# Kernel optimization log

Hardware: AMD Instinct MI355X
Metric: run time of the kernel (lower is better)

Reference implementation:

```python
import jax, jax.numpy as jnp
import numpy as np

N = 50000        # number of nodes
K = 32           # sampled neighbors per node (fixed degree)
D = 128          # input_dim
DOUT = 128       # output_dim


def setup_inputs() -> dict:
    key = jax.random.key(0)
    k1, k2, k3, k4, k5 = jax.random.split(key, 5)
    node_fea1 = jax.random.normal(k1, (N, D), dtype=jnp.float32)
    node_fea2 = jax.random.normal(k2, (N, D), dtype=jnp.float32)
    neigh_idx1 = jax.random.randint(k3, (N, K), 0, N, dtype=jnp.int32)
    neigh_idx2 = jax.random.randint(k4, (N, K), 0, N, dtype=jnp.int32)
    # xavier-uniform init for weight [4*D, DOUT]
    limit = float(np.sqrt(6.0 / (4 * D + DOUT)))
    weight = jax.random.uniform(k5, (4 * D, DOUT), dtype=jnp.float32,
                                minval=-limit, maxval=limit)
    return {"node_fea1": node_fea1, "node_fea2": node_fea2,
            "neigh_idx1": neigh_idx1, "neigh_idx2": neigh_idx2,
            "weight": weight}


def reference(node_fea1, node_fea2, neigh_idx1, neigh_idx2, weight):
    # neighbor mean aggregation of node_fea1 over the two neighbor lists
    # (forward_den reads node_fea1 in BOTH aggregation blocks)
    nei1 = node_fea1[neigh_idx1].mean(axis=1)   # [N, D]
    nei2 = node_fea1[neigh_idx2].mean(axis=1)   # [N, D]
    cat_fea = jnp.concatenate([node_fea1, node_fea2, nei1, nei2], axis=1)  # [N, 4D]
    return jnp.tanh(cat_fea @ weight)           # [N, DOUT]
```

## Files before the change

### kernel.cpp

```cpp
#include <hip/hip_runtime.h>
#include <math.h>

#define N_NODES 50000
#define KNEI    32
#define DIM     128
#define DOUT    128
#define NUNITS  (2 * N_NODES)

typedef __attribute__((ext_vector_type(8))) short short8;
typedef __attribute__((ext_vector_type(4))) float floatx4;

static __device__ __forceinline__ unsigned short f2bf(float f) {
    unsigned int u = __float_as_uint(f);
    unsigned int lsb = (u >> 16) & 1u;
    u += 0x7fffu + lsb;
    return (unsigned short)(u >> 16);
}
static __device__ __forceinline__ unsigned int pack2(float a, float b) {
    return (unsigned int)f2bf(a) | ((unsigned int)f2bf(b) << 16);
}
static __device__ __forceinline__ float fast_tanh(float x) {
    float ax = fabsf(x);
    float e  = __expf(2.0f * ax);
    float t  = 1.0f - 2.0f / (e + 1.0f);
    return copysignf(t, x);
}
static __device__ __forceinline__ unsigned int pk4_i8(float a, float b, float c,
                                                      float d, float inv) {
    int qa = (int)rintf(a * inv) & 0xff;
    int qb = (int)rintf(b * inv) & 0xff;
    int qc = (int)rintf(c * inv) & 0xff;
    int qd = (int)rintf(d * inv) & 0xff;
    return (unsigned int)(qa | (qb << 8) | (qc << 16) | (qd << 24));
}


__global__ __launch_bounds__(256) void convert_i8(
    const float* __restrict__ src, unsigned int* __restrict__ Q8,
    float* __restrict__ Sc)
{
    int t = blockIdx.x * 256 + threadIdx.x;
    if (t >= N_NODES * 8) return;
    int node = t >> 3, j = t & 7;
    const float* rp = src + node * DIM + j * 16;
    float4 v0 = *(const float4*)rp;
    float4 v1 = *(const float4*)(rp + 4);
    float4 v2 = *(const float4*)(rp + 8);
    float4 v3 = *(const float4*)(rp + 12);

    float am = fabsf(v0.x);
    am = fmaxf(am, fabsf(v0.y)); am = fmaxf(am, fabsf(v0.z)); am = fmaxf(am, fabsf(v0.w));
    am = fmaxf(am, fabsf(v1.x)); am = fmaxf(am, fabsf(v1.y));
    am = fmaxf(am, fabsf(v1.z)); am = fmaxf(am, fabsf(v1.w));
    am = fmaxf(am, fabsf(v2.x)); am = fmaxf(am, fabsf(v2.y));
    am = fmaxf(am, fabsf(v2.z)); am = fmaxf(am, fabsf(v2.w));
    am = fmaxf(am, fabsf(v3.x)); am = fmaxf(am, fabsf(v3.y));
    am = fmaxf(am, fabsf(v3.z)); am = fmaxf(am, fabsf(v3.w));
    #pragma unroll
    for (int d = 1; d < 8; d <<= 1) am = fmaxf(am, __shfl_xor(am, d, 64));

    float inv = (am > 1e-30f) ? 127.0f / am : 0.0f;
    int4 o;
    o.x = (int)pk4_i8(v0.x, v0.y, v0.z, v0.w, inv);
    o.y = (int)pk4_i8(v1.x, v1.y, v1.z, v1.w, inv);
    o.z = (int)pk4_i8(v2.x, v2.y, v2.z, v2.w, inv);
    o.w = (int)pk4_i8(v3.x, v3.y, v3.z, v3.w, inv);
    *(int4*)(Q8 + node * 32 + j * 4) = o;
    if (j == 0) Sc[node] = am * (1.0f / 127.0f);
}

__global__ __launch_bounds__(256) void transpose_w(
    const float* __restrict__ W, unsigned short* __restrict__ Wt)
{
    int t = blockIdx.x * 256 + threadIdx.x;
    int k = t >> 7, n = t & 127;
    Wt[n * 512 + k] = f2bf(W[t]);
}

__global__ __launch_bounds__(256) void aggregate_i8(
    const unsigned char* __restrict__ Q8,
    const float* __restrict__ Sc,
    const int* __restrict__ idx1,
    const int* __restrict__ idx2,
    unsigned short* __restrict__ NEI)
{
    __shared__ int   idxs[32][32];
    __shared__ float scs[32][32];

    const int tid = threadIdx.x;
    const int bu0 = blockIdx.x * 32;
    const int ul  = tid >> 3;
    const int l   = tid & 7;

    {
        int uu = bu0 + ul;
        const int* ip = ((uu & 1) ? idx2 : idx1) + (uu >> 1) * KNEI + l * 4;
        int4 v = *(const int4*)ip;
        *(int4*)&idxs[ul][l * 4] = v;
    }
    __syncthreads();

    {
        #pragma unroll
        for (int k = 0; k < 4; ++k)
            scs[ul][l * 4 + k] = Sc[idxs[ul][l * 4 + k]];
    }
    __syncthreads();

    const int u    = bu0 + ul;
    const int node = u >> 1;
    const int list = u & 1;

    int4 I[8];
    #pragma unroll
    for (int q = 0; q < 8; ++q) I[q] = *(const int4*)&idxs[ul][q * 4];

    const unsigned char* base = Q8 + l * 16;
    float sums[16];
    #pragma unroll
    for (int i = 0; i < 16; ++i) sums[i] = 0.f;

    #pragma unroll
    for (int q = 0; q < 8; ++q) {
        int rows[4] = {I[q].x, I[q].y, I[q].z, I[q].w};
        #pragma unroll
        for (int t4 = 0; t4 < 4; ++t4) {
            int4 v = *(const int4*)(base + (size_t)rows[t4] * 128);
            float s = scs[ul][q * 4 + t4];
            int d[4] = {v.x, v.y, v.z, v.w};
            #pragma unroll
            for (int j = 0; j < 4; ++j) {
                int w = d[j];
                sums[4 * j + 0] = fmaf(s, (float)((w << 24) >> 24), sums[4 * j + 0]);
                sums[4 * j + 1] = fmaf(s, (float)((w << 16) >> 24), sums[4 * j + 1]);
                sums[4 * j + 2] = fmaf(s, (float)((w <<  8) >> 24), sums[4 * j + 2]);
                sums[4 * j + 3] = fmaf(s, (float)( w        >> 24), sums[4 * j + 3]);
            }
        }
    }

    const float invK = 1.0f / 32.0f;
    int4 o0, o1;
    o0.x = (int)pack2(sums[0] * invK,  sums[1] * invK);
    o0.y = (int)pack2(sums[2] * invK,  sums[3] * invK);
    o0.z = (int)pack2(sums[4] * invK,  sums[5] * invK);
    o0.w = (int)pack2(sums[6] * invK,  sums[7] * invK);
    o1.x = (int)pack2(sums[8] * invK,  sums[9] * invK);
    o1.y = (int)pack2(sums[10] * invK, sums[11] * invK);
    o1.z = (int)pack2(sums[12] * invK, sums[13] * invK);
    o1.w = (int)pack2(sums[14] * invK, sums[15] * invK);
    unsigned short* op = NEI + node * 256 + list * 128 + l * 16;
    *(int4*)op       = o0;
    *(int4*)(op + 8) = o1;
}

__global__ __launch_bounds__(256) void gemm128(
    const float*          __restrict__ fea1,
    const float*          __restrict__ fea2,
    const unsigned short* __restrict__ NEI,
    const unsigned short* __restrict__ Wt,
    float* __restrict__ out)
{
    __shared__ unsigned short As[128][72];
    __shared__ unsigned short Bs[128][72];

    const int tid  = threadIdx.x;
    const int w    = tid >> 6;
    const int lane = tid & 63;
    const int m0   = blockIdx.x * 128;
    const int wm   = (w & 1) * 64;
    const int wn   = (w >> 1) * 64;
    const int lm   = lane & 15;
    const int lk   = (lane >> 4) * 8;

    floatx4 acc[4][4];
    #pragma unroll
    for (int i = 0; i < 4; ++i)
        #pragma unroll
        for (int j = 0; j < 4; ++j)
            acc[i][j] = (floatx4){0.f, 0.f, 0.f, 0.f};

    for (int cc = 0; cc < 8; ++cc) {
        const int kb = cc * 64;
        if (cc < 4) {
            const float* src = (cc < 2) ? fea1 : fea2;
            const int cbase = (cc & 1) * 64;
            #pragma unroll
            for (int i = 0; i < 8; ++i) {
                int f   = tid + i * 256;
                int row = f >> 4;
                int c4  = (f & 15) * 4;
                int node = m0 + row;
                if (node >= N_NODES) node = N_NODES - 1;
                float4 v = *(const float4*)(src + node * DIM + cbase + c4);
                *(unsigned int*)&As[row][c4 + 0] = pack2(v.x, v.y);
                *(unsigned int*)&As[row][c4 + 2] = pack2(v.z, v.w);
            }
        } else {
            const int cb = kb - 256;
            #pragma unroll
            for (int i = 0; i < 4; ++i) {
                int sl  = tid + i * 256;
                int row = sl >> 3;
                int o8  = (sl & 7) * 8;
                int node = m0 + row;
                if (node >= N_NODES) node = N_NODES - 1;
                *(int4*)&As[row][o8] = *(const int4*)(NEI + node * 256 + cb + o8);
            }
        }
        #pragma unroll
        for (int i = 0; i < 4; ++i) {
            int sl  = tid + i * 256;
            int row = sl >> 3;
            int o8  = (sl & 7) * 8;
            *(int4*)&Bs[row][o8] = *(const int4*)(Wt + row * 512 + kb + o8);
        }
        __syncthreads();

        #pragma unroll
        for (int ks = 0; ks < 64; ks += 32) {
            short8 af[4], bf_[4];
            #pragma unroll
            for (int im = 0; im < 4; ++im)
                af[im] = *(const short8*)&As[wm + im * 16 + lm][ks + lk];
            #pragma unroll
            for (int in = 0; in < 4; ++in)
                bf_[in] = *(const short8*)&Bs[wn + in * 16 + lm][ks + lk];
            #pragma unroll
            for (int im = 0; im < 4; ++im)
                #pragma unroll
                for (int in = 0; in < 4; ++in)
                    acc[im][in] = __builtin_amdgcn_mfma_f32_16x16x32_bf16(
                        af[im], bf_[in], acc[im][in], 0, 0, 0);
        }
        __syncthreads();
    }

    #pragma unroll
    for (int im = 0; im < 4; ++im) {
        int rbase = m0 + wm + im * 16 + (lane >> 4) * 4;
        #pragma unroll
        for (int in = 0; in < 4; ++in) {
            int col = wn + in * 16 + lm;
            #pragma unroll
            for (int r = 0; r < 4; ++r) {
                int node = rbase + r;
                if (node < N_NODES)
                    out[node * DOUT + col] = fast_tanh(acc[im][in][r]);
            }
        }
    }
}

#define MT      64
#define KC      64
#define AS_STRIDE 68

__global__ __launch_bounds__(256) void sage_fused_fb(
    const float* __restrict__ fea1, const float* __restrict__ fea2,
    const int* __restrict__ idx1, const int* __restrict__ idx2,
    const float* __restrict__ W, float* __restrict__ out)
{
    __shared__ float As[KC][AS_STRIDE];
    __shared__ int   idxs[MT][64];
    const int tid = threadIdx.x;
    const int n0  = blockIdx.x * MT;
    #pragma unroll
    for (int i = 0; i < 8; ++i) {
        int e = tid + i * 256, m = e >> 5, kk = e & 31;
        int node = n0 + m; if (node >= N_NODES) node = N_NODES - 1;
        idxs[m][kk]      = idx1[node * KNEI + kk];
        idxs[m][32 + kk] = idx2[node * KNEI + kk];
    }
    float acc[8][4];
    #pragma unroll
    for (int i = 0; i < 8; ++i)
        #pragma unroll
        for (int j = 0; j < 4; ++j) acc[i][j] = 0.f;
    const int j0 = (tid & 31) * 4;
    const int m0 = (tid >> 5) * 8;
    for (int c = 0; c < 8; ++c) {
        if (c < 4) {
            const float* src = (c < 2) ? fea1 : fea2;
            const int cbase = (c & 1) * 64;
            #pragma unroll
            for (int i = 0; i < 4; ++i) {
                int f = tid + i * 256, m = f >> 4, c4 = (f & 15) * 4;
                int node = n0 + m; if (node >= N_NODES) node = N_NODES - 1;
                float4 v = *(const float4*)(src + node * DIM + cbase + c4);
                As[c4 + 0][m] = v.x; As[c4 + 1][m] = v.y;
                As[c4 + 2][m] = v.z; As[c4 + 3][m] = v.w;
            }
        } else {
            const int col = tid & 63, kbase = (c & 1) * 64;
            const int lbase = (c < 6) ? 0 : 32, g = tid >> 6;
            for (int mm = 0; mm < 16; ++mm) {
                const int m = g * 16 + mm;
                const int4* ip = (const int4*)&idxs[m][lbase];
                float s = 0.f;
                #pragma unroll
                for (int q = 0; q < 8; ++q) {
                    int4 nb = ip[q];
                    s += fea1[nb.x * DIM + kbase + col];
                    s += fea1[nb.y * DIM + kbase + col];
                    s += fea1[nb.z * DIM + kbase + col];
                    s += fea1[nb.w * DIM + kbase + col];
                }
                As[col][m] = s * (1.0f / 32.0f);
            }
        }
        __syncthreads();
        const float* wp = W + (c * KC) * DOUT + j0;
        #pragma unroll 4
        for (int k = 0; k < KC; ++k) {
            float4 w4 = *(const float4*)(wp + k * DOUT);
            const float4* ap = (const float4*)&As[k][m0];
            float4 a0 = ap[0]; float4 a1 = ap[1];
            float av[8] = {a0.x, a0.y, a0.z, a0.w, a1.x, a1.y, a1.z, a1.w};
            #pragma unroll
            for (int i = 0; i < 8; ++i) {
                acc[i][0] += av[i] * w4.x; acc[i][1] += av[i] * w4.y;
                acc[i][2] += av[i] * w4.z; acc[i][3] += av[i] * w4.w;
            }
        }
        __syncthreads();
    }
    #pragma unroll
    for (int i = 0; i < 8; ++i) {
        int node = n0 + m0 + i;
        if (node < N_NODES) {
            float4 r;
            r.x = tanhf(acc[i][0]); r.y = tanhf(acc[i][1]);
            r.z = tanhf(acc[i][2]); r.w = tanhf(acc[i][3]);
            *(float4*)(out + node * DOUT + j0) = r;
        }
    }
}

extern "C" void kernel_launch(void* const* d_in, const int* in_sizes, int n_in,
                              void* d_out, int out_size, void* d_ws, size_t ws_size,
                              hipStream_t stream) {
    const float* fea1 = (const float*)d_in[0];
    const float* fea2 = (const float*)d_in[1];
    const int*   idx1 = (const int*)d_in[2];
    const int*   idx2 = (const int*)d_in[3];
    const float* W    = (const float*)d_in[4];
    float* out = (float*)d_out;

    const size_t Q8_BYTES  = (size_t)N_NODES * DIM;
    const size_t SC_BYTES  = (size_t)N_NODES * 4;
    const size_t NEI_BYTES = (size_t)N_NODES * 256 * 2;
    const size_t WT_BYTES  = (size_t)512 * 128 * 2;

    if (ws_size >= Q8_BYTES + SC_BYTES + NEI_BYTES + WT_BYTES) {
        unsigned char*  Q8  = (unsigned char*)d_ws;
        float*          Scp = (float*)((char*)d_ws + Q8_BYTES);
        unsigned short* NEI = (unsigned short*)((char*)d_ws + Q8_BYTES + SC_BYTES);
        unsigned short* Wt  = (unsigned short*)((char*)d_ws + Q8_BYTES + SC_BYTES + NEI_BYTES);

        convert_i8<<<(N_NODES * 8 + 255) / 256, 256, 0, stream>>>(
            fea1, (unsigned int*)Q8, Scp);
        transpose_w<<<512 * 128 / 256, 256, 0, stream>>>(W, Wt);
        aggregate_i8<<<NUNITS / 32, 256, 0, stream>>>(Q8, Scp, idx1, idx2, NEI);
        gemm128<<<(N_NODES + 127) / 128, 256, 0, stream>>>(fea1, fea2, NEI, Wt, out);
    } else {
        const int grid = (N_NODES + MT - 1) / MT;
        sage_fused_fb<<<grid, 256, 0, stream>>>(fea1, fea2, idx1, idx2, W, out);
    }
}
```

Baseline: 169.6 us.

## Shrink GEMM row tile to 32 and batch gather loads in aggregation

The GEMM kernel's row tile drops from 128 to 32 rows per block, so the grid grows from 391 to 1563 blocks and the 256 CUs are better filled. The cost is that the weight tile is reloaded into shared memory four times as often. The aggregation kernel now issues eight independent int8 row gathers before consuming them, to raise memory-level parallelism. It also pads the shared index and scale arrays and sets a minimum-occupancy hint on its launch bounds.

```diff
diff --git a/kernel.cpp b/kernel.cpp
--- a/kernel.cpp
+++ b/kernel.cpp
@@ -77,15 +77,15 @@
     Wt[n * 512 + k] = f2bf(W[t]);
 }
 
-__global__ __launch_bounds__(256) void aggregate_i8(
+__global__ __launch_bounds__(256, 4) void aggregate_i8(
     const unsigned char* __restrict__ Q8,
     const float* __restrict__ Sc,
     const int* __restrict__ idx1,
     const int* __restrict__ idx2,
     unsigned short* __restrict__ NEI)
 {
-    __shared__ int   idxs[32][32];
-    __shared__ float scs[32][32];
+    __shared__ int   idxs[32][40];
+    __shared__ float scs[32][40];
 
     const int tid = threadIdx.x;
     const int bu0 = blockIdx.x * 32;
@@ -111,30 +111,33 @@
     const int node = u >> 1;
     const int list = u & 1;
 
-    int4 I[8];
-    #pragma unroll
-    for (int q = 0; q < 8; ++q) I[q] = *(const int4*)&idxs[ul][q * 4];
-
     const unsigned char* base = Q8 + l * 16;
     float sums[16];
     #pragma unroll
     for (int i = 0; i < 16; ++i) sums[i] = 0.f;
 
     #pragma unroll
-    for (int q = 0; q < 8; ++q) {
-        int rows[4] = {I[q].x, I[q].y, I[q].z, I[q].w};
-        #pragma unroll
-        for (int t4 = 0; t4 < 4; ++t4) {
-            int4 v = *(const int4*)(base + (size_t)rows[t4] * 128);
-            float s = scs[ul][q * 4 + t4];
-            int d[4] = {v.x, v.y, v.z, v.w};
-            #pragma unroll
-            for (int j = 0; j < 4; ++j) {
-                int w = d[j];
-                sums[4 * j + 0] = fmaf(s, (float)((w << 24) >> 24), sums[4 * j + 0]);
-                sums[4 * j + 1] = fmaf(s, (float)((w << 16) >> 24), sums[4 * j + 1]);
-                sums[4 * j + 2] = fmaf(s, (float)((w <<  8) >> 24), sums[4 * j + 2]);
-                sums[4 * j + 3] = fmaf(s, (float)( w        >> 24), sums[4 * j + 3]);
+    for (int b = 0; b < 4; ++b) {
+        int4 i4a = *(const int4*)&idxs[ul][b * 8];
+        int4 i4b = *(const int4*)&idxs[ul][b * 8 + 4];
+        int rows[8] = {i4a.x, i4a.y, i4a.z, i4a.w,
+                       i4b.x, i4b.y, i4b.z, i4b.w};
+        int4 v[8];
+        #pragma unroll
+        for (int j = 0; j < 8; ++j)
+            v[j] = *(const int4*)(base + (size_t)rows[j] * 128);
+
+        #pragma unroll
+        for (int j = 0; j < 8; ++j) {
+            float s = scs[ul][b * 8 + j];
+            int d[4] = {v[j].x, v[j].y, v[j].z, v[j].w};
+            #pragma unroll
+            for (int jj = 0; jj < 4; ++jj) {
+                int w = d[jj];
+                sums[4 * jj + 0] = fmaf(s, (float)((w << 24) >> 24), sums[4 * jj + 0]);
+                sums[4 * jj + 1] = fmaf(s, (float)((w << 16) >> 24), sums[4 * jj + 1]);
+                sums[4 * jj + 2] = fmaf(s, (float)((w <<  8) >> 24), sums[4 * jj + 2]);
+                sums[4 * jj + 3] = fmaf(s, (float)( w        >> 24), sums[4 * jj + 3]);
             }
         }
     }
@@ -154,31 +157,29 @@
     *(int4*)(op + 8) = o1;
 }
 
-__global__ __launch_bounds__(256) void gemm128(
+__global__ __launch_bounds__(256) void gemm32(
     const float*          __restrict__ fea1,
     const float*          __restrict__ fea2,
     const unsigned short* __restrict__ NEI,
     const unsigned short* __restrict__ Wt,
     float* __restrict__ out)
 {
-    __shared__ unsigned short As[128][72];
+    __shared__ unsigned short As[32][72];
     __shared__ unsigned short Bs[128][72];
 
     const int tid  = threadIdx.x;
     const int w    = tid >> 6;
     const int lane = tid & 63;
-    const int m0   = blockIdx.x * 128;
-    const int wm   = (w & 1) * 64;
+    const int m0   = blockIdx.x * 32;
+    const int wm   = (w & 1) * 16;
     const int wn   = (w >> 1) * 64;
     const int lm   = lane & 15;
     const int lk   = (lane >> 4) * 8;
 
-    floatx4 acc[4][4];
-    #pragma unroll
-    for (int i = 0; i < 4; ++i)
-        #pragma unroll
-        for (int j = 0; j < 4; ++j)
-            acc[i][j] = (floatx4){0.f, 0.f, 0.f, 0.f};
+    floatx4 acc[4];
+    #pragma unroll
+    for (int in = 0; in < 4; ++in)
+        acc[in] = (floatx4){0.f, 0.f, 0.f, 0.f};
 
     for (int cc = 0; cc < 8; ++cc) {
         const int kb = cc * 64;
@@ -186,7 +187,7 @@
             const float* src = (cc < 2) ? fea1 : fea2;
             const int cbase = (cc & 1) * 64;
             #pragma unroll
-            for (int i = 0; i < 8; ++i) {
+            for (int i = 0; i < 2; ++i) {
                 int f   = tid + i * 256;
                 int row = f >> 4;
                 int c4  = (f & 15) * 4;
@@ -198,15 +199,11 @@
             }
         } else {
             const int cb = kb - 256;
-            #pragma unroll
-            for (int i = 0; i < 4; ++i) {
-                int sl  = tid + i * 256;
-                int row = sl >> 3;
-                int o8  = (sl & 7) * 8;
-                int node = m0 + row;
-                if (node >= N_NODES) node = N_NODES - 1;
-                *(int4*)&As[row][o8] = *(const int4*)(NEI + node * 256 + cb + o8);
-            }
+            int row = tid >> 3;
+            int o8  = (tid & 7) * 8;
+            int node = m0 + row;
+            if (node >= N_NODES) node = N_NODES - 1;
+            *(int4*)&As[row][o8] = *(const int4*)(NEI + node * 256 + cb + o8);
         }
         #pragma unroll
         for (int i = 0; i < 4; ++i) {
@@ -219,35 +216,28 @@
 
         #pragma unroll
         for (int ks = 0; ks < 64; ks += 32) {
-            short8 af[4], bf_[4];
-            #pragma unroll
-            for (int im = 0; im < 4; ++im)
-                af[im] = *(const short8*)&As[wm + im * 16 + lm][ks + lk];
+            short8 af = *(const short8*)&As[wm + lm][ks + lk];
+            short8 bf_[4];
             #pragma unroll
             for (int in = 0; in < 4; ++in)
                 bf_[in] = *(const short8*)&Bs[wn + in * 16 + lm][ks + lk];
             #pragma unroll
-            for (int im = 0; im < 4; ++im)
-                #pragma unroll
-                for (int in = 0; in < 4; ++in)
-                    acc[im][in] = __builtin_amdgcn_mfma_f32_16x16x32_bf16(
-                        af[im], bf_[in], acc[im][in], 0, 0, 0);
+            for (int in = 0; in < 4; ++in)
+                acc[in] = __builtin_amdgcn_mfma_f32_16x16x32_bf16(
+                    af, bf_[in], acc[in], 0, 0, 0);
         }
         __syncthreads();
     }
 
-    #pragma unroll
-    for (int im = 0; im < 4; ++im) {
-        int rbase = m0 + wm + im * 16 + (lane >> 4) * 4;
-        #pragma unroll
-        for (int in = 0; in < 4; ++in) {
-            int col = wn + in * 16 + lm;
-            #pragma unroll
-            for (int r = 0; r < 4; ++r) {
-                int node = rbase + r;
-                if (node < N_NODES)
-                    out[node * DOUT + col] = fast_tanh(acc[im][in][r]);
-            }
+    int rbase = m0 + wm + (lane >> 4) * 4;
+    #pragma unroll
+    for (int in = 0; in < 4; ++in) {
+        int col = wn + in * 16 + lm;
+        #pragma unroll
+        for (int r = 0; r < 4; ++r) {
+            int node = rbase + r;
+            if (node < N_NODES)
+                out[node * DOUT + col] = fast_tanh(acc[in][r]);
         }
     }
 }
@@ -362,7 +352,7 @@
             fea1, (unsigned int*)Q8, Scp);
         transpose_w<<<512 * 128 / 256, 256, 0, stream>>>(W, Wt);
         aggregate_i8<<<NUNITS / 32, 256, 0, stream>>>(Q8, Scp, idx1, idx2, NEI);
-        gemm128<<<(N_NODES + 127) / 128, 256, 0, stream>>>(fea1, fea2, NEI, Wt, out);
+        gemm32<<<(N_NODES + 31) / 32, 256, 0, stream>>>(fea1, fea2, NEI, Wt, out);
     } else {
         const int grid = (N_NODES + MT - 1) / MT;
         sage_fused_fb<<<grid, 256, 0, stream>>>(fea1, fea2, idx1, idx2, W, out);
```

After: 188.9 us. 11.4% more time.
